# Optimization experiments

Hardware: AMD Instinct MI355X
Metric: run time of the kernel (lower is better)

The kernel has to match this reference:

```python
import jax, jax.numpy as jnp
import numpy as np

N_NODES = 50000
N_EDGES = 800000
NH, FOUT, FIN = 4, 32, 128
LEAKY_SLOPE = 0.2


def setup_inputs() -> dict:
    key = jax.random.key(0)
    k1, k2, k3, k4, k5 = jax.random.split(key, 5)
    x = jax.random.normal(k1, (N_NODES, FIN), dtype=jnp.float32)
    edge_index = jax.random.randint(k2, (2, N_EDGES), 0, N_NODES, dtype=jnp.int64)
    W = jax.random.normal(k3, (FIN, NH * FOUT), dtype=jnp.float32) * (1.0 / np.sqrt(FIN))
    a_src = jax.random.normal(k4, (NH, FOUT), dtype=jnp.float32)
    a_trg = jax.random.normal(k5, (NH, FOUT), dtype=jnp.float32)
    bias = jnp.zeros((NH * FOUT,), dtype=jnp.float32)
    return {"x": x, "edge_index": edge_index, "W": W, "a_src": a_src, "a_trg": a_trg, "bias": bias}


def reference(x, edge_index, W, a_src, a_trg, bias):
    N = x.shape[0]
    # Step 1: linear projection (dropout omitted: eval mode)
    proj = (x @ W).reshape(N, NH, FOUT)              # (N, NH, FOUT)
    # Per-head attention scores for each node as source / target
    s_src = jnp.einsum('nhf,hf->nh', proj, a_src)    # (N, NH)
    s_trg = jnp.einsum('nhf,hf->nh', proj, a_trg)    # (N, NH)
    # Step 2: lift to edges (gather) and score
    src, trg = edge_index[0], edge_index[1]
    e = jax.nn.leaky_relu(s_src[src] + s_trg[trg], LEAKY_SLOPE)   # (E, NH)
    # Step 3: neighborhood-aware softmax (global max shift, as in GAT imp3)
    exp_e = jnp.exp(e - e.max())                      # (E, NH)
    denom = jax.ops.segment_sum(exp_e, trg, num_segments=N)       # (N, NH)
    att = exp_e / (denom[trg] + 1e-16)                # (E, NH)
    # Step 4: weight lifted source features and scatter-aggregate to targets
    weighted = proj[src] * att[:, :, None]            # (E, NH, FOUT)
    out = jax.ops.segment_sum(weighted, trg, num_segments=N)      # (N, NH, FOUT)
    # Step 5: skip connection (FIN == NH*FOUT -> direct add), concat heads, bias, ELU
    out = out + x.reshape(N, NH, FOUT)
    out = out.reshape(N, NH * FOUT) + bias
    return jax.nn.elu(out)
```

## Files before the change

### kernel.cpp

```cpp
#include <hip/hip_runtime.h>
#include <stdint.h>

typedef __attribute__((ext_vector_type(8))) short short8;
typedef __attribute__((ext_vector_type(4))) float floatx4;

__device__ inline float bf2f(unsigned short b) {
    unsigned u = ((unsigned)b) << 16;
    return __builtin_bit_cast(float, u);
}
__device__ inline unsigned short f2bf(float f) {
    unsigned u = __builtin_bit_cast(unsigned, f);
    unsigned r = (u + 0x7fffu + ((u >> 16) & 1u)) >> 16;
    return (unsigned short)r;
}
__device__ inline float ldf(const void* p, int i, int f32) {
    return f32 ? ((const float*)p)[i] : bf2f(((const unsigned short*)p)[i]);
}
__device__ inline int lde(const int* ei, int idx, int is64) {
    return is64 ? ei[2 * idx] : ei[idx];
}

__global__ void k_det(const void* x, const int* ei, int* flags) {
    __shared__ int h1, h2;
    if (threadIdx.x == 0) { h1 = 0; h2 = 0; }
    __syncthreads();
    const unsigned short* xs = (const unsigned short*)x;
    int c1 = 0;
    for (int i = threadIdx.x * 2; i < 65536; i += 512)
        if ((xs[i] & 0x7f80u) == 0x7f80u) c1++;
    int c2 = 0;
    for (int i = threadIdx.x * 2 + 1; i < 8192; i += 512)
        if (ei[i] != 0) c2++;
    atomicAdd(&h1, c1);
    atomicAdd(&h2, c2);
    __syncthreads();
    if (threadIdx.x == 0) { flags[0] = (h1 >= 8); flags[1] = (h2 < 8); }
}

__global__ void k0_init(int* counts, int* cursor, int N) {
    int i = blockIdx.x * blockDim.x + threadIdx.x;
    if (i <= N) counts[i] = 0;
    if (i < N) cursor[i] = 0;
}

__global__ __launch_bounds__(256) void k_conv(
    const void* __restrict__ W, const int* __restrict__ flags,
    unsigned short* __restrict__ WhT, unsigned short* __restrict__ WlT)
{
    int f32 = flags[0];
    int idx = blockIdx.x * 256 + threadIdx.x;
    if (idx >= 128 * 128) return;
    int n = idx >> 7, k = idx & 127;
    float v = ldf(W, k * 128 + n, f32);
    unsigned short h = f2bf(v);
    WhT[idx] = h;
    WlT[idx] = f2bf(v - bf2f(h));
}

__global__ __launch_bounds__(256) void k1_gemm(
    const void* __restrict__ x, const unsigned short* __restrict__ WhT,
    const unsigned short* __restrict__ WlT, const void* __restrict__ a_src,
    const void* __restrict__ a_trg, const int* __restrict__ flags,
    unsigned short* __restrict__ projb, float* __restrict__ ssrc,
    float* __restrict__ strg, int N)
{
    __shared__ __align__(16) unsigned short WT[128 * 136];
    int t = threadIdx.x;
    int f32 = flags[0];
    for (int i = t; i < 2048; i += 256) {
        int row = i >> 4, ch = (i & 15) * 8;
        *(short8*)&WT[row * 136 + ch] = *(const short8*)&WhT[row * 128 + ch];
    }
    __syncthreads();
    int wave = t >> 6, lane = t & 63;
    int col = lane & 15, quad = lane >> 4;
    int row0 = blockIdx.x * 64 + wave * 16;
    int m = row0 + col;
    if (m >= N) m = N - 1;
    short8 ah[4], al[4];
    if (f32) {
        const float* xf = (const float*)x + (size_t)m * 128 + quad * 8;
#pragma unroll
        for (int kb = 0; kb < 4; kb++) {
            float4 v0 = *(const float4*)(xf + kb * 32);
            float4 v1 = *(const float4*)(xf + kb * 32 + 4);
            float vv[8] = {v0.x, v0.y, v0.z, v0.w, v1.x, v1.y, v1.z, v1.w};
#pragma unroll
            for (int j = 0; j < 8; j++) {
                unsigned short h = f2bf(vv[j]);
                ah[kb][j] = (short)h;
                al[kb][j] = (short)f2bf(vv[j] - bf2f(h));
            }
        }
    } else {
        const unsigned short* xb = (const unsigned short*)x + (size_t)m * 128 + quad * 8;
#pragma unroll
        for (int kb = 0; kb < 4; kb++)
            ah[kb] = *(const short8*)(xb + kb * 32);
    }
    floatx4 acc[8];
#pragma unroll
    for (int c = 0; c < 8; c++) acc[c] = (floatx4){0.f, 0.f, 0.f, 0.f};
#pragma unroll
    for (int c = 0; c < 8; c++) {
        const short8* bp = (const short8*)(&WT[(c * 16 + col) * 136 + quad * 8]);
        short8 b0 = bp[0], b1 = bp[4], b2 = bp[8], b3 = bp[12];
        acc[c] = __builtin_amdgcn_mfma_f32_16x16x32_bf16(ah[0], b0, acc[c], 0, 0, 0);
        acc[c] = __builtin_amdgcn_mfma_f32_16x16x32_bf16(ah[1], b1, acc[c], 0, 0, 0);
        acc[c] = __builtin_amdgcn_mfma_f32_16x16x32_bf16(ah[2], b2, acc[c], 0, 0, 0);
        acc[c] = __builtin_amdgcn_mfma_f32_16x16x32_bf16(ah[3], b3, acc[c], 0, 0, 0);
        if (f32) {
            acc[c] = __builtin_amdgcn_mfma_f32_16x16x32_bf16(al[0], b0, acc[c], 0, 0, 0);
            acc[c] = __builtin_amdgcn_mfma_f32_16x16x32_bf16(al[1], b1, acc[c], 0, 0, 0);
            acc[c] = __builtin_amdgcn_mfma_f32_16x16x32_bf16(al[2], b2, acc[c], 0, 0, 0);
            acc[c] = __builtin_amdgcn_mfma_f32_16x16x32_bf16(al[3], b3, acc[c], 0, 0, 0);
        }
    }
    if (f32) {
        __syncthreads();
        for (int i = t; i < 2048; i += 256) {
            int row = i >> 4, ch = (i & 15) * 8;
            *(short8*)&WT[row * 136 + ch] = *(const short8*)&WlT[row * 128 + ch];
        }
        __syncthreads();
#pragma unroll
        for (int c = 0; c < 8; c++) {
            const short8* bp = (const short8*)(&WT[(c * 16 + col) * 136 + quad * 8]);
            acc[c] = __builtin_amdgcn_mfma_f32_16x16x32_bf16(ah[0], bp[0], acc[c], 0, 0, 0);
            acc[c] = __builtin_amdgcn_mfma_f32_16x16x32_bf16(ah[1], bp[4], acc[c], 0, 0, 0);
            acc[c] = __builtin_amdgcn_mfma_f32_16x16x32_bf16(ah[2], bp[8], acc[c], 0, 0, 0);
            acc[c] = __builtin_amdgcn_mfma_f32_16x16x32_bf16(ah[3], bp[12], acc[c], 0, 0, 0);
        }
    }
#pragma unroll
    for (int r = 0; r < 4; r++) {
        int row = row0 + quad * 4 + r;
        if (row < N) {
#pragma unroll
            for (int c = 0; c < 8; c++)
                projb[(size_t)row * 128 + c * 16 + col] = f2bf(acc[c][r]);
        }
    }
    float asv[8], atv[8];
#pragma unroll
    for (int c = 0; c < 8; c++) {
        int j = c * 16 + col;
        asv[c] = ldf(a_src, j, f32);
        atv[c] = ldf(a_trg, j, f32);
    }
#pragma unroll
    for (int r = 0; r < 4; r++) {
        int row = row0 + quad * 4 + r;
        float ps[4] = {0.f, 0.f, 0.f, 0.f}, pt[4] = {0.f, 0.f, 0.f, 0.f};
#pragma unroll
        for (int c = 0; c < 8; c++) {
            int h = c >> 1;
            ps[h] += acc[c][r] * asv[c];
            pt[h] += acc[c][r] * atv[c];
        }
#pragma unroll
        for (int k = 1; k < 16; k <<= 1) {
#pragma unroll
            for (int h = 0; h < 4; h++) {
                ps[h] += __shfl_xor(ps[h], k, 16);
                pt[h] += __shfl_xor(pt[h], k, 16);
            }
        }
        if (col == 0 && row < N) {
#pragma unroll
            for (int h = 0; h < 4; h++) {
                ssrc[(size_t)row * 4 + h] = ps[h];
                strg[(size_t)row * 4 + h] = pt[h];
            }
        }
    }
}

__device__ inline void edge_scores(const float* ssrc, const float* strg,
                                   int src, int trg, float* v) {
    float4 a = *(const float4*)(ssrc + (size_t)src * 4);
    float4 b = *(const float4*)(strg + (size_t)trg * 4);
    v[0] = a.x + b.x; v[1] = a.y + b.y; v[2] = a.z + b.z; v[3] = a.w + b.w;
#pragma unroll
    for (int h = 0; h < 4; h++) v[h] = v[h] > 0.f ? v[h] : 0.2f * v[h];
}

__global__ __launch_bounds__(256) void kE_count_max(
    const int* __restrict__ ei, const float* __restrict__ ssrc,
    const float* __restrict__ strg, const int* __restrict__ flags,
    int* __restrict__ counts, float* __restrict__ blockmax, int E, int N)
{
    int e64 = flags[1];
    int e = blockIdx.x * 256 + threadIdx.x;
    float m = -3.0e38f;
    if (e < E) {
        int src = min(max(lde(ei, e, e64), 0), N - 1);
        int trg = min(max(lde(ei, E + e, e64), 0), N - 1);
        atomicAdd(&counts[trg], 1);
        float v[4];
        edge_scores(ssrc, strg, src, trg, v);
        m = fmaxf(fmaxf(v[0], v[1]), fmaxf(v[2], v[3]));
    }
#pragma unroll
    for (int k = 1; k < 64; k <<= 1) m = fmaxf(m, __shfl_xor(m, k, 64));
    __shared__ float wm[4];
    if ((threadIdx.x & 63) == 0) wm[threadIdx.x >> 6] = m;
    __syncthreads();
    if (threadIdx.x == 0)
        blockmax[blockIdx.x] = fmaxf(fmaxf(wm[0], wm[1]), fmaxf(wm[2], wm[3]));
}

__global__ __launch_bounds__(256) void kS1_psum(
    const int* __restrict__ counts, int* __restrict__ partials, int NP1)
{
    int idx = blockIdx.x * 256 + threadIdx.x;
    int v = (idx < NP1) ? counts[idx] : 0;
#pragma unroll
    for (int k = 1; k < 64; k <<= 1) v += __shfl_xor(v, k, 64);
    __shared__ int wsum[4];
    if ((threadIdx.x & 63) == 0) wsum[threadIdx.x >> 6] = v;
    __syncthreads();
    if (threadIdx.x == 0)
        partials[blockIdx.x] = wsum[0] + wsum[1] + wsum[2] + wsum[3];
}

__global__ __launch_bounds__(256) void kS2_scanp(
    int* __restrict__ partials, int nb,
    const float* __restrict__ blockmax, float* __restrict__ Mval, int nbm)
{
    int t = threadIdx.x;
    if (nb <= 256) {
        __shared__ int lds[256];
        int v = (t < nb) ? partials[t] : 0;
        lds[t] = v;
        __syncthreads();
        int incl = v;
        for (int st = 1; st < 256; st <<= 1) {
            int add = (t >= st) ? lds[t - st] : 0;
            __syncthreads();
            incl += add;
            lds[t] = incl;
            __syncthreads();
        }
        if (t < nb) partials[t] = incl - v;
    } else if (t == 0) {
        int run = 0;
        for (int i = 0; i < nb; i++) { int c = partials[i]; partials[i] = run; run += c; }
    }
    __syncthreads();
    float m = -3.0e38f;
    for (int i = t; i < nbm; i += 256) m = fmaxf(m, blockmax[i]);
#pragma unroll
    for (int k = 1; k < 64; k <<= 1) m = fmaxf(m, __shfl_xor(m, k, 64));
    __shared__ float wm[4];
    if ((t & 63) == 0) wm[t >> 6] = m;
    __syncthreads();
    if (t == 0) *Mval = fmaxf(fmaxf(wm[0], wm[1]), fmaxf(wm[2], wm[3]));
}

__global__ __launch_bounds__(256) void kS3_offs(
    const int* __restrict__ counts, const int* __restrict__ partials,
    int* __restrict__ offsets, int NP1)
{
    int t = threadIdx.x;
    int idx = blockIdx.x * 256 + t;
    int v = (idx < NP1) ? counts[idx] : 0;
    __shared__ int lds[256];
    lds[t] = v;
    __syncthreads();
    int incl = v;
    for (int st = 1; st < 256; st <<= 1) {
        int add = (t >= st) ? lds[t - st] : 0;
        __syncthreads();
        incl += add;
        lds[t] = incl;
        __syncthreads();
    }
    if (idx < NP1) offsets[idx] = partials[blockIdx.x] + incl - v;
}

__global__ __launch_bounds__(256) void k2c_scatter_exp(
    const int* __restrict__ ei, const int* __restrict__ offsets,
    const float* __restrict__ ssrc, const float* __restrict__ strg,
    const int* __restrict__ flags, const float* __restrict__ Mval,
    int* __restrict__ cursor, int* __restrict__ esrc, float4* __restrict__ eexp,
    int E, int N)
{
    int e64 = flags[1];
    int e = blockIdx.x * 256 + threadIdx.x;
    if (e >= E) return;
    float M = *Mval;
    int src = min(max(lde(ei, e, e64), 0), N - 1);
    int trg = min(max(lde(ei, E + e, e64), 0), N - 1);
    int pos = offsets[trg] + atomicAdd(&cursor[trg], 1);
    if (pos < 0 || pos >= E) return;
    esrc[pos] = src;
    float v[4];
    edge_scores(ssrc, strg, src, trg, v);
    eexp[pos] = make_float4(__expf(v[0] - M), __expf(v[1] - M),
                            __expf(v[2] - M), __expf(v[3] - M));
}

__global__ __launch_bounds__(256) void k2c_scatter(
    const int* __restrict__ ei, const int* __restrict__ offsets,
    const int* __restrict__ flags, int* __restrict__ cursor,
    int* __restrict__ esrc, int E, int N)
{
    int e64 = flags[1];
    int e = blockIdx.x * 256 + threadIdx.x;
    if (e >= E) return;
    int src = min(max(lde(ei, e, e64), 0), N - 1);
    int trg = min(max(lde(ei, E + e, e64), 0), N - 1);
    int pos = offsets[trg] + atomicAdd(&cursor[trg], 1);
    if (pos >= 0 && pos < E) esrc[pos] = src;
}

__global__ __launch_bounds__(256) void k3_agg_e(
    const int* __restrict__ offsets, const int* __restrict__ esrc,
    const float4* __restrict__ eexp, const unsigned short* __restrict__ projb,
    const void* __restrict__ x, const void* __restrict__ bias,
    const int* __restrict__ flags, float* __restrict__ out, int N, int E)
{
    int w = threadIdx.x >> 6;
    int lane = threadIdx.x & 63;
    int n = blockIdx.x * 4 + w;
    int f32 = flags[0];
    bool valid = (n < N);
    int nc = valid ? n : N - 1;
    int off = offsets[nc];
    int d = offsets[nc + 1] - off;
    d = max(0, min(d, E));
    if (!valid) d = 0;

    float den[4] = {0.f, 0.f, 0.f, 0.f};
    for (int i = lane; i < d; i += 64) {
        float4 ev = eexp[off + i];
        den[0] += ev.x; den[1] += ev.y; den[2] += ev.z; den[3] += ev.w;
    }
#pragma unroll
    for (int k = 1; k < 64; k <<= 1)
#pragma unroll
        for (int h = 0; h < 4; h++) den[h] += __shfl_xor(den[h], k, 64);
    float inv[4];
#pragma unroll
    for (int h = 0; h < 4; h++) inv[h] = 1.0f / (den[h] + 1e-16f);

    __shared__ int dmax_s[4];
    if (lane == 0) dmax_s[w] = d;
    __syncthreads();
    int dmx = max(max(dmax_s[0], dmax_s[1]), max(dmax_s[2], dmax_s[3]));

    __shared__ int lsrc[4][64];
    __shared__ float latt[4][64 * 5];
    float acc0 = 0.f, acc1 = 0.f;
    int h01 = lane >> 4;
    for (int base = 0; base < dmx; base += 64) {
        int cd = min(64, d - base);
        if (lane < cd) {
            int s = min(max(esrc[off + base + lane], 0), N - 1);
            lsrc[w][lane] = s;
            float4 ev = eexp[off + base + lane];
            latt[w][lane * 5 + 0] = ev.x * inv[0];
            latt[w][lane * 5 + 1] = ev.y * inv[1];
            latt[w][lane * 5 + 2] = ev.z * inv[2];
            latt[w][lane * 5 + 3] = ev.w * inv[3];
        }
        __syncthreads();
        for (int k = 0; k < cd; k++) {
            int s = lsrc[w][k];
            float att = latt[w][k * 5 + h01];
            unsigned p = *(const unsigned*)(projb + (size_t)s * 128 + lane * 2);
            acc0 = fmaf(bf2f((unsigned short)(p & 0xffffu)), att, acc0);
            acc1 = fmaf(bf2f((unsigned short)(p >> 16)), att, acc1);
        }
        __syncthreads();
    }

    if (!valid) return;
    int j0 = lane * 2;
    float o0 = acc0 + ldf(x, n * 128 + j0, f32) + ldf(bias, j0, f32);
    float o1 = acc1 + ldf(x, n * 128 + j0 + 1, f32) + ldf(bias, j0 + 1, f32);
    o0 = o0 > 0.f ? o0 : __expf(o0) - 1.f;
    o1 = o1 > 0.f ? o1 : __expf(o1) - 1.f;
    out[(size_t)n * 128 + j0]     = o0;
    out[(size_t)n * 128 + j0 + 1] = o1;
}

__global__ __launch_bounds__(256) void k3_agg_g(
    const int* __restrict__ offsets, const int* __restrict__ esrc,
    const float* __restrict__ ssrc, const float* __restrict__ strg,
    const unsigned short* __restrict__ projb, const void* __restrict__ x,
    const void* __restrict__ bias, const int* __restrict__ flags,
    const float* __restrict__ Mval, float* __restrict__ out, int N, int E)
{
    int w = threadIdx.x >> 6;
    int lane = threadIdx.x & 63;
    int n = blockIdx.x * 4 + w;
    int f32 = flags[0];
    bool valid = (n < N);
    int nc = valid ? n : N - 1;
    int off = offsets[nc];
    int d = offsets[nc + 1] - off;
    d = max(0, min(d, E));
    if (!valid) d = 0;
    float M = *Mval;
    float4 stv = *(const float4*)(strg + (size_t)nc * 4);
    float st[4] = {stv.x, stv.y, stv.z, stv.w};
    float den[4] = {0.f, 0.f, 0.f, 0.f};
    for (int i = lane; i < d; i += 64) {
        int s = min(max(esrc[off + i], 0), N - 1);
        float4 ssv = *(const float4*)(ssrc + (size_t)s * 4);
        float sv[4] = {ssv.x, ssv.y, ssv.z, ssv.w};
#pragma unroll
        for (int h = 0; h < 4; h++) {
            float v = sv[h] + st[h];
            v = v > 0.f ? v : 0.2f * v;
            den[h] += __expf(v - M);
        }
    }
#pragma unroll
    for (int k = 1; k < 64; k <<= 1)
#pragma unroll
        for (int h = 0; h < 4; h++) den[h] += __shfl_xor(den[h], k, 64);
    float inv[4];
#pragma unroll
    for (int h = 0; h < 4; h++) inv[h] = 1.0f / (den[h] + 1e-16f);
    __shared__ int dmax_s[4];
    if (lane == 0) dmax_s[w] = d;
    __syncthreads();
    int dmx = max(max(dmax_s[0], dmax_s[1]), max(dmax_s[2], dmax_s[3]));
    __shared__ int lsrc[4][64];
    __shared__ float latt[4][64 * 5];
    float acc0 = 0.f, acc1 = 0.f;
    int h01 = lane >> 4;
    for (int base = 0; base < dmx; base += 64) {
        int cd = min(64, d - base);
        if (lane < cd) {
            int s = min(max(esrc[off + base + lane], 0), N - 1);
            lsrc[w][lane] = s;
            float4 ssv = *(const float4*)(ssrc + (size_t)s * 4);
            float sv[4] = {ssv.x, ssv.y, ssv.z, ssv.w};
#pragma unroll
            for (int h = 0; h < 4; h++) {
                float v = sv[h] + st[h];
                v = v > 0.f ? v : 0.2f * v;
                latt[w][lane * 5 + h] = __expf(v - M) * inv[h];
            }
        }
        __syncthreads();
        for (int k = 0; k < cd; k++) {
            int s = lsrc[w][k];
            float att = latt[w][k * 5 + h01];
            unsigned p = *(const unsigned*)(projb + (size_t)s * 128 + lane * 2);
            acc0 = fmaf(bf2f((unsigned short)(p & 0xffffu)), att, acc0);
            acc1 = fmaf(bf2f((unsigned short)(p >> 16)), att, acc1);
        }
        __syncthreads();
    }
    if (!valid) return;
    int j0 = lane * 2;
    float o0 = acc0 + ldf(x, n * 128 + j0, f32) + ldf(bias, j0, f32);
    float o1 = acc1 + ldf(x, n * 128 + j0 + 1, f32) + ldf(bias, j0 + 1, f32);
    o0 = o0 > 0.f ? o0 : __expf(o0) - 1.f;
    o1 = o1 > 0.f ? o1 : __expf(o1) - 1.f;
    out[(size_t)n * 128 + j0]     = o0;
    out[(size_t)n * 128 + j0 + 1] = o1;
}

extern "C" void kernel_launch(void* const* d_in, const int* in_sizes, int n_in,
                              void* d_out, int out_size, void* d_ws, size_t ws_size,
                              hipStream_t stream)
{
    const void* x     = d_in[0];
    const int*  ei    = (const int*)d_in[1];
    const void* W     = d_in[2];
    const void* a_src = d_in[3];
    const void* a_trg = d_in[4];
    const void* bias  = d_in[5];
    float* out = (float*)d_out;
    int N = in_sizes[0] / 128;
    int E = N * 16;
    if (in_sizes[1] / 2 < E) E = in_sizes[1] / 2;
    int nbE = (E + 255) / 256;
    int NP1 = N + 1;
    int nbS = (NP1 + 255) / 256;

    char* ws = (char*)d_ws;
    size_t o = 0;
    auto alloc = [&](size_t bytes) {
        size_t r = o;
        o = (o + bytes + 255) & ~(size_t)255;
        return r;
    };
    int* flags = (int*)(ws + alloc(256));
    unsigned short* projb = (unsigned short*)(ws + alloc((size_t)N * 128 * 2));
    float* ssrc  = (float*)(ws + alloc((size_t)N * 4 * 4));
    float* strg  = (float*)(ws + alloc((size_t)N * 4 * 4));
    float* Mval  = (float*)(ws + alloc(256));
    int* counts  = (int*)(ws + alloc((size_t)NP1 * 4));
    int* offsets = (int*)(ws + alloc((size_t)NP1 * 4));
    int* cursor  = (int*)(ws + alloc((size_t)N * 4));
    int* esrc    = (int*)(ws + alloc((size_t)E * 4));
    float* blockmax = (float*)(ws + alloc((size_t)nbE * 4));
    int* partials = (int*)(ws + alloc((size_t)nbS * 4));
    unsigned short* WhT = (unsigned short*)(ws + alloc(128 * 128 * 2));
    unsigned short* WlT = (unsigned short*)(ws + alloc(128 * 128 * 2));
    size_t base = o;
    size_t need_eexp = base + (size_t)E * 16 + 256;

    k_det<<<1, 256, 0, stream>>>(x, ei, flags);
    k0_init<<<(N + 256) / 256, 256, 0, stream>>>(counts, cursor, N);
    k_conv<<<64, 256, 0, stream>>>(W, flags, WhT, WlT);
    k1_gemm<<<(N + 63) / 64, 256, 0, stream>>>(x, WhT, WlT, a_src, a_trg, flags,
                                               projb, ssrc, strg, N);
    kE_count_max<<<nbE, 256, 0, stream>>>(ei, ssrc, strg, flags, counts, blockmax, E, N);
    kS1_psum<<<nbS, 256, 0, stream>>>(counts, partials, NP1);
    kS2_scanp<<<1, 256, 0, stream>>>(partials, nbS, blockmax, Mval, nbE);
    kS3_offs<<<nbS, 256, 0, stream>>>(counts, partials, offsets, NP1);

    if (ws_size >= need_eexp) {
        float4* eexp = (float4*)(ws + alloc((size_t)E * 16));
        k2c_scatter_exp<<<nbE, 256, 0, stream>>>(ei, offsets, ssrc, strg, flags, Mval,
                                                 cursor, esrc, eexp, E, N);
        k3_agg_e<<<(N + 3) / 4, 256, 0, stream>>>(offsets, esrc, eexp, projb, x, bias,
                                                  flags, out, N, E);
    } else {
        k2c_scatter<<<nbE, 256, 0, stream>>>(ei, offsets, flags, cursor, esrc, E, N);
        k3_agg_g<<<(N + 3) / 4, 256, 0, stream>>>(offsets, esrc, ssrc, strg, projb, x, bias,
                                                  flags, Mval, out, N, E);
    }
}
```

Measured before the change: 268.2 us.

## Fold softmax denominator into single aggregation pass and drop per-edge exp buffer

Removes the path that precomputed per-edge exp scores into a float4 workspace buffer. The aggregation kernel now computes exp scores on the fly and accumulates the unnormalized weighted sum and the denominator in the same loop, normalizing once at the end. This removes the separate denominator pass and the E×16-byte eexp write and read, at the cost of recomputing exp per edge and gathering ssrc inside the main loop. Normalizing after accumulation changes the floating-point rounding slightly.

```diff
diff --git a/kernel.cpp b/kernel.cpp
--- a/kernel.cpp
+++ b/kernel.cpp
@@ -279,28 +279,6 @@
     if (idx < NP1) offsets[idx] = partials[blockIdx.x] + incl - v;
 }
 
-__global__ __launch_bounds__(256) void k2c_scatter_exp(
-    const int* __restrict__ ei, const int* __restrict__ offsets,
-    const float* __restrict__ ssrc, const float* __restrict__ strg,
-    const int* __restrict__ flags, const float* __restrict__ Mval,
-    int* __restrict__ cursor, int* __restrict__ esrc, float4* __restrict__ eexp,
-    int E, int N)
-{
-    int e64 = flags[1];
-    int e = blockIdx.x * 256 + threadIdx.x;
-    if (e >= E) return;
-    float M = *Mval;
-    int src = min(max(lde(ei, e, e64), 0), N - 1);
-    int trg = min(max(lde(ei, E + e, e64), 0), N - 1);
-    int pos = offsets[trg] + atomicAdd(&cursor[trg], 1);
-    if (pos < 0 || pos >= E) return;
-    esrc[pos] = src;
-    float v[4];
-    edge_scores(ssrc, strg, src, trg, v);
-    eexp[pos] = make_float4(__expf(v[0] - M), __expf(v[1] - M),
-                            __expf(v[2] - M), __expf(v[3] - M));
-}
-
 __global__ __launch_bounds__(256) void k2c_scatter(
     const int* __restrict__ ei, const int* __restrict__ offsets,
     const int* __restrict__ flags, int* __restrict__ cursor,
@@ -315,78 +293,7 @@
     if (pos >= 0 && pos < E) esrc[pos] = src;
 }
 
-__global__ __launch_bounds__(256) void k3_agg_e(
-    const int* __restrict__ offsets, const int* __restrict__ esrc,
-    const float4* __restrict__ eexp, const unsigned short* __restrict__ projb,
-    const void* __restrict__ x, const void* __restrict__ bias,
-    const int* __restrict__ flags, float* __restrict__ out, int N, int E)
-{
-    int w = threadIdx.x >> 6;
-    int lane = threadIdx.x & 63;
-    int n = blockIdx.x * 4 + w;
-    int f32 = flags[0];
-    bool valid = (n < N);
-    int nc = valid ? n : N - 1;
-    int off = offsets[nc];
-    int d = offsets[nc + 1] - off;
-    d = max(0, min(d, E));
-    if (!valid) d = 0;
-
-    float den[4] = {0.f, 0.f, 0.f, 0.f};
-    for (int i = lane; i < d; i += 64) {
-        float4 ev = eexp[off + i];
-        den[0] += ev.x; den[1] += ev.y; den[2] += ev.z; den[3] += ev.w;
-    }
-#pragma unroll
-    for (int k = 1; k < 64; k <<= 1)
-#pragma unroll
-        for (int h = 0; h < 4; h++) den[h] += __shfl_xor(den[h], k, 64);
-    float inv[4];
-#pragma unroll
-    for (int h = 0; h < 4; h++) inv[h] = 1.0f / (den[h] + 1e-16f);
-
-    __shared__ int dmax_s[4];
-    if (lane == 0) dmax_s[w] = d;
-    __syncthreads();
-    int dmx = max(max(dmax_s[0], dmax_s[1]), max(dmax_s[2], dmax_s[3]));
-
-    __shared__ int lsrc[4][64];
-    __shared__ float latt[4][64 * 5];
-    float acc0 = 0.f, acc1 = 0.f;
-    int h01 = lane >> 4;
-    for (int base = 0; base < dmx; base += 64) {
-        int cd = min(64, d - base);
-        if (lane < cd) {
-            int s = min(max(esrc[off + base + lane], 0), N - 1);
-            lsrc[w][lane] = s;
-            float4 ev = eexp[off + base + lane];
-            latt[w][lane * 5 + 0] = ev.x * inv[0];
-            latt[w][lane * 5 + 1] = ev.y * inv[1];
-            latt[w][lane * 5 + 2] = ev.z * inv[2];
-            latt[w][lane * 5 + 3] = ev.w * inv[3];
-        }
-        __syncthreads();
-        for (int k = 0; k < cd; k++) {
-            int s = lsrc[w][k];
-            float att = latt[w][k * 5 + h01];
-            unsigned p = *(const unsigned*)(projb + (size_t)s * 128 + lane * 2);
-            acc0 = fmaf(bf2f((unsigned short)(p & 0xffffu)), att, acc0);
-            acc1 = fmaf(bf2f((unsigned short)(p >> 16)), att, acc1);
-        }
-        __syncthreads();
-    }
-
-    if (!valid) return;
-    int j0 = lane * 2;
-    float o0 = acc0 + ldf(x, n * 128 + j0, f32) + ldf(bias, j0, f32);
-    float o1 = acc1 + ldf(x, n * 128 + j0 + 1, f32) + ldf(bias, j0 + 1, f32);
-    o0 = o0 > 0.f ? o0 : __expf(o0) - 1.f;
-    o1 = o1 > 0.f ? o1 : __expf(o1) - 1.f;
-    out[(size_t)n * 128 + j0]     = o0;
-    out[(size_t)n * 128 + j0 + 1] = o1;
-}
-
-__global__ __launch_bounds__(256) void k3_agg_g(
+__global__ __launch_bounds__(256) void k3_agg(
     const int* __restrict__ offsets, const int* __restrict__ esrc,
     const float* __restrict__ ssrc, const float* __restrict__ strg,
     const unsigned short* __restrict__ projb, const void* __restrict__ x,
@@ -406,31 +313,15 @@
     float M = *Mval;
     float4 stv = *(const float4*)(strg + (size_t)nc * 4);
     float st[4] = {stv.x, stv.y, stv.z, stv.w};
-    float den[4] = {0.f, 0.f, 0.f, 0.f};
-    for (int i = lane; i < d; i += 64) {
-        int s = min(max(esrc[off + i], 0), N - 1);
-        float4 ssv = *(const float4*)(ssrc + (size_t)s * 4);
-        float sv[4] = {ssv.x, ssv.y, ssv.z, ssv.w};
-#pragma unroll
-        for (int h = 0; h < 4; h++) {
-            float v = sv[h] + st[h];
-            v = v > 0.f ? v : 0.2f * v;
-            den[h] += __expf(v - M);
-        }
-    }
-#pragma unroll
-    for (int k = 1; k < 64; k <<= 1)
-#pragma unroll
-        for (int h = 0; h < 4; h++) den[h] += __shfl_xor(den[h], k, 64);
-    float inv[4];
-#pragma unroll
-    for (int h = 0; h < 4; h++) inv[h] = 1.0f / (den[h] + 1e-16f);
+
     __shared__ int dmax_s[4];
     if (lane == 0) dmax_s[w] = d;
     __syncthreads();
     int dmx = max(max(dmax_s[0], dmax_s[1]), max(dmax_s[2], dmax_s[3]));
+
     __shared__ int lsrc[4][64];
     __shared__ float latt[4][64 * 5];
+    float den[4] = {0.f, 0.f, 0.f, 0.f};
     float acc0 = 0.f, acc1 = 0.f;
     int h01 = lane >> 4;
     for (int base = 0; base < dmx; base += 64) {
@@ -444,19 +335,29 @@
             for (int h = 0; h < 4; h++) {
                 float v = sv[h] + st[h];
                 v = v > 0.f ? v : 0.2f * v;
-                latt[w][lane * 5 + h] = __expf(v - M) * inv[h];
+                float ev = __expf(v - M);
+                latt[w][lane * 5 + h] = ev;
+                den[h] += ev;
             }
         }
         __syncthreads();
         for (int k = 0; k < cd; k++) {
             int s = lsrc[w][k];
-            float att = latt[w][k * 5 + h01];
+            float ev = latt[w][k * 5 + h01];
             unsigned p = *(const unsigned*)(projb + (size_t)s * 128 + lane * 2);
-            acc0 = fmaf(bf2f((unsigned short)(p & 0xffffu)), att, acc0);
-            acc1 = fmaf(bf2f((unsigned short)(p >> 16)), att, acc1);
-        }
-        __syncthreads();
-    }
+            acc0 = fmaf(bf2f((unsigned short)(p & 0xffffu)), ev, acc0);
+            acc1 = fmaf(bf2f((unsigned short)(p >> 16)), ev, acc1);
+        }
+        __syncthreads();
+    }
+#pragma unroll
+    for (int k = 1; k < 64; k <<= 1)
+#pragma unroll
+        for (int h = 0; h < 4; h++) den[h] += __shfl_xor(den[h], k, 64);
+    float inv = 1.0f / (den[h01] + 1e-16f);
+    acc0 *= inv;
+    acc1 *= inv;
+
     if (!valid) return;
     int j0 = lane * 2;
     float o0 = acc0 + ldf(x, n * 128 + j0, f32) + ldf(bias, j0, f32);
@@ -505,8 +406,6 @@
     int* partials = (int*)(ws + alloc((size_t)nbS * 4));
     unsigned short* WhT = (unsigned short*)(ws + alloc(128 * 128 * 2));
     unsigned short* WlT = (unsigned short*)(ws + alloc(128 * 128 * 2));
-    size_t base = o;
-    size_t need_eexp = base + (size_t)E * 16 + 256;
 
     k_det<<<1, 256, 0, stream>>>(x, ei, flags);
     k0_init<<<(N + 256) / 256, 256, 0, stream>>>(counts, cursor, N);
@@ -517,16 +416,7 @@
     kS1_psum<<<nbS, 256, 0, stream>>>(counts, partials, NP1);
     kS2_scanp<<<1, 256, 0, stream>>>(partials, nbS, blockmax, Mval, nbE);
     kS3_offs<<<nbS, 256, 0, stream>>>(counts, partials, offsets, NP1);
-
-    if (ws_size >= need_eexp) {
-        float4* eexp = (float4*)(ws + alloc((size_t)E * 16));
-        k2c_scatter_exp<<<nbE, 256, 0, stream>>>(ei, offsets, ssrc, strg, flags, Mval,
-                                                 cursor, esrc, eexp, E, N);
-        k3_agg_e<<<(N + 3) / 4, 256, 0, stream>>>(offsets, esrc, eexp, projb, x, bias,
-                                                  flags, out, N, E);
-    } else {
-        k2c_scatter<<<nbE, 256, 0, stream>>>(ei, offsets, flags, cursor, esrc, E, N);
-        k3_agg_g<<<(N + 3) / 4, 256, 0, stream>>>(offsets, esrc, ssrc, strg, projb, x, bias,
-                                                  flags, Mval, out, N, E);
-    }
-}
+    k2c_scatter<<<nbE, 256, 0, stream>>>(ei, offsets, flags, cursor, esrc, E, N);
+    k3_agg<<<(N + 3) / 4, 256, 0, stream>>>(offsets, esrc, ssrc, strg, projb, x, bias,
+                                            flags, Mval, out, N, E);
+}
```

After: 267.0 us. No clear change (-0.4%).
